# Kernel tuning notes

Measured on AMD Instinct MI355X. Metric: run time of the kernel, lower is better.

Reference implementation:

```python
import jax, jax.numpy as jnp
import numpy as np

DIM = 1024
HEADS = 16
DIM_HEAD = 64
INNER = HEADS * DIM_HEAD  # 1024
SCALE = DIM_HEAD ** -0.5


def setup_inputs() -> dict:
    key = jax.random.key(0)
    ks = jax.random.split(key, 5)
    B, N = 4, 2048
    x = jax.random.normal(ks[0], (B, N, DIM), dtype=jnp.float32)
    # torch Linear weights are [out, in]; store transposed [in, out] for x @ W
    s = 1.0 / np.sqrt(DIM)
    Wq = jax.random.uniform(ks[1], (DIM, INNER), minval=-s, maxval=s, dtype=jnp.float32)
    Wkv = jax.random.uniform(ks[2], (DIM, 2 * INNER), minval=-s, maxval=s, dtype=jnp.float32)
    so = 1.0 / np.sqrt(INNER)
    Wo = jax.random.uniform(ks[3], (INNER, DIM), minval=-so, maxval=so, dtype=jnp.float32)
    bo = jax.random.uniform(ks[4], (DIM,), minval=-so, maxval=so, dtype=jnp.float32)
    return {"x": x, "Wq": Wq, "Wkv": Wkv, "Wo": Wo, "bo": bo}


def reference(x, Wq, Wkv, Wo, bo):
    B, N, _ = x.shape
    q = x @ Wq                      # [B, N, INNER]
    kv = x @ Wkv                    # [B, N, 2*INNER]
    k, v = jnp.split(kv, 2, axis=-1)

    def split_heads(t):
        return t.reshape(B, N, HEADS, DIM_HEAD).transpose(0, 2, 1, 3)  # [B,H,N,D]

    q, k, v = split_heads(q) * SCALE, split_heads(k), split_heads(v)
    sim = jnp.einsum('bhid,bhjd->bhij', q, k)  # [B,H,N,N]
    mask_value = -jnp.finfo(sim.dtype).max
    # causal: mask strictly-upper triangle (triu with offset j-i+1 = 1)
    causal_mask = jnp.triu(jnp.ones((N, N), dtype=bool), k=1)
    sim = jnp.where(causal_mask[None, None, :, :], mask_value, sim)
    attn = jax.nn.softmax(sim, axis=-1)
    out = jnp.einsum('bhij,bhjd->bhid', attn, v)            # [B,H,N,D]
    out = out.transpose(0, 2, 1, 3).reshape(B, N, INNER)    # [B,N,INNER]
    return out @ Wo + bo
```

## Files before the change

### kernel.cpp

```cpp
#include <hip/hip_runtime.h>

typedef unsigned short u16;
typedef __bf16 bf16x8 __attribute__((ext_vector_type(8)));
typedef float floatx4 __attribute__((ext_vector_type(4)));
typedef unsigned as1_u32 __attribute__((address_space(1)));
typedef unsigned as3_u32 __attribute__((address_space(3)));

__device__ inline u16 f2bf(float f) {
    unsigned int u = __builtin_bit_cast(unsigned int, f);
    u += 0x7fffu + ((u >> 16) & 1u);
    return (u16)(u >> 16);
}
__device__ inline floatx4 mfma16(bf16x8 a, bf16x8 b, floatx4 c) {
    return __builtin_amdgcn_mfma_f32_16x16x32_bf16(a, b, c, 0, 0, 0);
}
__device__ inline void gld16(const u16* g, u16* l) {
    __builtin_amdgcn_global_load_lds((const as1_u32*)g, (as3_u32*)l, 16, 0, 0);
}
__device__ inline unsigned permpack(float lo, float hi) {
    return __builtin_amdgcn_perm(__builtin_bit_cast(unsigned, hi),
                                 __builtin_bit_cast(unsigned, lo), 0x07060302u);
}

#define NSEQ 2048
#define DIM  1024
#define HEADS 16
#define DHEAD 64
#define QSCALE 0.18033688f
#define CSHIFT 4.328085f

__device__ inline void transpose_tile(const float* __restrict__ src,
                                      u16* __restrict__ dst, int ncols,
                                      int n0, int k0, int t) {
    __shared__ u16 tile[64][72];
    #pragma unroll
    for (int rr = 0; rr < 4; rr++) {
        const int k = (t >> 4) + rr * 16;
        const int n = (t & 15) * 4;
        float4 v = *(const float4*)&src[(size_t)(k0 + k) * ncols + n0 + n];
        tile[n + 0][k] = f2bf(v.x); tile[n + 1][k] = f2bf(v.y);
        tile[n + 2][k] = f2bf(v.z); tile[n + 3][k] = f2bf(v.w);
    }
    __syncthreads();
    #pragma unroll
    for (int ww = 0; ww < 2; ww++) {
        const int idx = t + ww * 256;
        const int n = idx >> 3, g = idx & 7;
        u16 tmp[8] __attribute__((aligned(16)));
        #pragma unroll
        for (int i = 0; i < 8; i++) tmp[i] = tile[n][g * 8 + i];
        *(uint4*)&dst[(size_t)(n0 + n) * 1024 + k0 + g * 8] = *(const uint4*)tmp;
    }
}

__global__ __launch_bounds__(256) void prep_fused(
    const float* __restrict__ x,  u16* __restrict__ xb,
    const float* __restrict__ Wq, const float* __restrict__ Wkv,
    u16* __restrict__ Wt)
{
    const int bid = blockIdx.x;
    const int t = threadIdx.x;
    if (bid < 4096) {
        const size_t i = ((size_t)bid * 256 + t) * 8;
        float4 a = *(const float4*)&x[i];
        float4 b = *(const float4*)&x[i + 4];
        u16 o[8] __attribute__((aligned(16)));
        o[0] = f2bf(a.x); o[1] = f2bf(a.y); o[2] = f2bf(a.z); o[3] = f2bf(a.w);
        o[4] = f2bf(b.x); o[5] = f2bf(b.y); o[6] = f2bf(b.z); o[7] = f2bf(b.w);
        *(uint4*)&xb[i] = *(const uint4*)o;
    } else if (bid < 4352) {
        const int v = bid - 4096;
        transpose_tile(Wq, Wt, 1024, (v & 15) * 64, (v >> 4) * 64, t);
    } else {
        const int v = bid - 4352;
        transpose_tile(Wkv, Wt + (size_t)1024 * 1024, 2048, (v & 31) * 64, (v >> 5) * 64, t);
    }
}

__global__ __launch_bounds__(256) void transpose_conv(const float* __restrict__ src,
                                                      u16* __restrict__ dst, int ncols) {
    transpose_tile(src, dst, ncols, blockIdx.x * 64, blockIdx.y * 64, threadIdx.x);
}

__global__ __launch_bounds__(256) void qkv_gemm_v3(
    const u16* __restrict__ xb, const u16* __restrict__ Wt,
    u16* __restrict__ q_ws, u16* __restrict__ k_ws, u16* __restrict__ v_ws)
{
    __shared__ u16 a0[128 * 32], a1[128 * 32];
    __shared__ u16 b0[128 * 32], b1[128 * 32];

    const int n0 = blockIdx.x * 128;
    const int m0 = blockIdx.y * 128;
    const int t = threadIdx.x, lane = t & 63, w = t >> 6;
    const int wr = w >> 1, wc = w & 1;
    const int quad = lane >> 4, l16 = lane & 15;
    const int lrow = lane >> 2, lk = (lane & 3) * 8;

    floatx4 acc[4][4];
    #pragma unroll
    for (int i = 0; i < 4; i++)
        #pragma unroll
        for (int j = 0; j < 4; j++) acc[i][j] = floatx4{0.f, 0.f, 0.f, 0.f};

    for (int k0 = 0; k0 < DIM; k0 += 64) {
        __syncthreads();
        #pragma unroll
        for (int hh = 0; hh < 2; hh++) {
            const int row = w * 32 + hh * 16;
            const size_t ga = (size_t)(m0 + row + lrow) * DIM + k0 + lk;
            const size_t gb = (size_t)(n0 + row + lrow) * DIM + k0 + lk;
            gld16(&xb[ga],      &a0[row * 32]);
            gld16(&xb[ga + 32], &a1[row * 32]);
            gld16(&Wt[gb],      &b0[row * 32]);
            gld16(&Wt[gb + 32], &b1[row * 32]);
        }
        __syncthreads();

        #pragma unroll
        for (int ks = 0; ks < 2; ks++) {
            const u16* al = ks ? a1 : a0;
            const u16* bl = ks ? b1 : b0;
            bf16x8 af[4], bf[4];
            #pragma unroll
            for (int i = 0; i < 4; i++)
                af[i] = *(const bf16x8*)&al[(wr * 64 + i * 16 + l16) * 32 + quad * 8];
            #pragma unroll
            for (int j = 0; j < 4; j++)
                bf[j] = *(const bf16x8*)&bl[(wc * 64 + j * 16 + l16) * 32 + quad * 8];
            #pragma unroll
            for (int i = 0; i < 4; i++)
                #pragma unroll
                for (int j = 0; j < 4; j++)
                    acc[i][j] = mfma16(af[i], bf[j], acc[i][j]);
        }
    }

    const int seg = n0 >> 10;
    #pragma unroll
    for (int j = 0; j < 4; j++) {
        const int n  = n0 + wc * 64 + j * 16 + l16;
        const int nn = n & 1023;
        const int h  = nn >> 6, d = nn & 63;
        #pragma unroll
        for (int i = 0; i < 4; i++) {
            const int mb = m0 + wr * 64 + i * 16 + quad * 4;
            const int b = mb >> 11, ib = mb & (NSEQ - 1);
            if (seg == 0) {
                #pragma unroll
                for (int r = 0; r < 4; r++)
                    q_ws[(((size_t)(b * HEADS + h)) * NSEQ + ib + r) * DHEAD + d] =
                        f2bf(acc[i][j][r] * QSCALE);
            } else if (seg == 1) {
                #pragma unroll
                for (int r = 0; r < 4; r++)
                    k_ws[(((size_t)(b * HEADS + h)) * NSEQ + ib + r) * DHEAD + d] =
                        f2bf(acc[i][j][r]);
            } else {
                u16 tmp[4] __attribute__((aligned(8)));
                #pragma unroll
                for (int r = 0; r < 4; r++) tmp[r] = f2bf(acc[i][j][r]);
                *(uint2*)&v_ws[(((size_t)(b * HEADS + h)) * DHEAD + d) * NSEQ + ib] =
                    *(const uint2*)tmp;
            }
        }
    }
}

__global__ __launch_bounds__(256) void attn_v8(
    const u16* __restrict__ q_ws, const u16* __restrict__ k_ws,
    const u16* __restrict__ v_ws, u16* __restrict__ attn_ws)
{
    __shared__ u16 kds[2][64 * 64];
    __shared__ u16 vds[2][64 * 64];
    __shared__ u16 p_lds[4 * 2048];

    const int bid = blockIdx.x;
    const int bh  = bid & 63;
    const int t16 = 15 - (bid >> 6);
    const int i0  = t16 * 128;
    const int b   = bh >> 4, h = bh & 15;

    const u16* qb = q_ws + (size_t)bh * NSEQ * DHEAD;
    const u16* kb = k_ws + (size_t)bh * NSEQ * DHEAD;
    const u16* vb = v_ws + (size_t)bh * DHEAD * NSEQ;

    const int t    = threadIdx.x;
    const int lane = t & 63, w = t >> 6;
    const int quad = lane >> 4, l16 = lane & 15;

    const int srow8 = lane >> 3;
    const int chunk = (lane & 7) ^ srow8;
    const int krow  = w * 16 + srow8;
    const size_t koff = (size_t)krow * DHEAD + chunk * 8;
    const size_t voff = (size_t)krow * NSEQ + chunk * 8;
    u16* klbase = (u16*)&kds[0][0] + w * 1024;
    u16* vlbase = (u16*)&vds[0][0] + w * 1024;
    const int sw = (l16 & 7);

    bf16x8 qf[2][2];
    #pragma unroll
    for (int rf = 0; rf < 2; rf++)
        #pragma unroll
        for (int dg = 0; dg < 2; dg++)
            qf[rf][dg] = *(const bf16x8*)&qb[(size_t)(i0 + rf * 64 + w * 16 + l16) * DHEAD
                                             + dg * 32 + quad * 8];

    floatx4 l4[2] = {floatx4{0.f,0.f,0.f,0.f}, floatx4{0.f,0.f,0.f,0.f}};
    floatx4 acc[2][4];
    #pragma unroll
    for (int rf = 0; rf < 2; rf++)
        #pragma unroll
        for (int dg = 0; dg < 4; dg++) acc[rf][dg] = floatx4{0.f, 0.f, 0.f, 0.f};

    const int jt_max = 2 * t16 + 1;

    gld16(&kb[koff],             klbase);
    gld16(&kb[koff + 8 * DHEAD], klbase + 512);
    gld16(&vb[voff],             vlbase);
    gld16(&vb[voff + 8 * NSEQ],  vlbase + 512);

    for (int jt = 0; jt <= jt_max; jt++) {
        const int cur = jt & 1;
        __syncthreads();

        if (jt < jt_max) {
            const size_t j64 = (size_t)(jt + 1) * 64;
            const int nb = (cur ^ 1) * 4096;
            gld16(&kb[j64 * DHEAD + koff],             klbase + nb);
            gld16(&kb[j64 * DHEAD + koff + 8 * DHEAD], klbase + nb + 512);
            gld16(&vb[j64 + voff],                     vlbase + nb);
            gld16(&vb[j64 + voff + 8 * NSEQ],          vlbase + nb + 512);
        }

        const u16* kl = &kds[cur][0];
        const u16* vl = &vds[cur][0];
        const int j0 = jt * 64;

        floatx4 s[2][4];
        #pragma unroll
        for (int rf = 0; rf < 2; rf++)
            #pragma unroll
            for (int g = 0; g < 4; g++)
                s[rf][g] = floatx4{-CSHIFT, -CSHIFT, -CSHIFT, -CSHIFT};
        __builtin_amdgcn_s_setprio(1);
        #pragma unroll
        for (int dg = 0; dg < 2; dg++)
            #pragma unroll
            for (int g = 0; g < 4; g++) {
                bf16x8 kf = *(const bf16x8*)&kl[(g * 16 + l16) * 64
                                                + (((dg * 4 + quad) ^ sw) * 8)];
                s[0][g] = mfma16(kf, qf[0][dg], s[0][g]);
                s[1][g] = mfma16(kf, qf[1][dg], s[1][g]);
            }
        __builtin_amdgcn_s_setprio(0);

        #pragma unroll
        for (int rf = 0; rf < 2; rf++) {
            const int imin = i0 + rf * 64 + w * 16;
            if (j0 + 63 > imin) {
                const int i = imin + l16;
                #pragma unroll
                for (int g = 0; g < 4; g++) {
                    const int jb = j0 + g * 16 + quad * 4;
                    #pragma unroll
                    for (int r = 0; r < 4; r++)
                        if (jb + r > i) s[rf][g][r] = -1e30f;
                }
            }
        }

        #pragma unroll
        for (int rf = 0; rf < 2; rf++) {
            #pragma unroll
            for (int g = 0; g < 4; g++) {
                #pragma unroll
                for (int r = 0; r < 4; r++)
                    s[rf][g][r] = __builtin_amdgcn_exp2f(s[rf][g][r]);
                l4[rf] += s[rf][g];
                uint2 pk;
                pk.x = permpack(s[rf][g][0], s[rf][g][1]);
                pk.y = permpack(s[rf][g][2], s[rf][g][3]);
                const int c = 2 * g + (quad >> 1);
                *(uint2*)&p_lds[w * 2048 + rf * 1024 + (c >> 2) * 512 + (c & 3) * 128
                                + l16 * 8 + (quad & 1) * 4] = pk;
            }
        }
        asm volatile("s_waitcnt lgkmcnt(0)" ::: "memory");

        __builtin_amdgcn_s_setprio(1);
        #pragma unroll
        for (int jg = 0; jg < 2; jg++) {
            bf16x8 pf0 = *(const bf16x8*)&p_lds[w * 2048 + jg * 512 + quad * 128 + l16 * 8];
            bf16x8 pf1 = *(const bf16x8*)&p_lds[w * 2048 + 1024 + jg * 512 + quad * 128 + l16 * 8];
            #pragma unroll
            for (int dg = 0; dg < 4; dg++) {
                bf16x8 vf = *(const bf16x8*)&vl[(dg * 16 + l16) * 64
                                                + (((jg * 4 + quad) ^ sw) * 8)];
                acc[0][dg] = mfma16(pf0, vf, acc[0][dg]);
                acc[1][dg] = mfma16(pf1, vf, acc[1][dg]);
            }
        }
        __builtin_amdgcn_s_setprio(0);
    }

    #pragma unroll
    for (int rf = 0; rf < 2; rf++) {
        float l_ln = (l4[rf][0] + l4[rf][1]) + (l4[rf][2] + l4[rf][3]);
        l_ln += __shfl_xor(l_ln, 16);
        l_ln += __shfl_xor(l_ln, 32);
        float linv[4];
        #pragma unroll
        for (int r = 0; r < 4; r++)
            linv[r] = 1.0f / __shfl(l_ln, quad * 4 + r);
        #pragma unroll
        for (int dg = 0; dg < 4; dg++)
            #pragma unroll
            for (int r = 0; r < 4; r++) {
                const float o = acc[rf][dg][r] * linv[r];
                const int i = i0 + rf * 64 + w * 16 + quad * 4 + r;
                attn_ws[(((size_t)(b * NSEQ + i)) * HEADS + h) * DHEAD + dg * 16 + l16] =
                    f2bf(o);
            }
    }
}

__global__ __launch_bounds__(256) void out_gemm_v3(
    const u16* __restrict__ attn, const u16* __restrict__ Wot,
    const float* __restrict__ bo, float* __restrict__ out)
{
    __shared__ u16 a0[128 * 32], a1[128 * 32];
    __shared__ u16 b0[128 * 32], b1[128 * 32];

    const int n0 = blockIdx.x * 128;
    const int m0 = blockIdx.y * 128;
    const int t = threadIdx.x, lane = t & 63, w = t >> 6;
    const int wr = w >> 1, wc = w & 1;
    const int quad = lane >> 4, l16 = lane & 15;
    const int lrow = lane >> 2, lk = (lane & 3) * 8;

    floatx4 acc[4][4];
    #pragma unroll
    for (int i = 0; i < 4; i++)
        #pragma unroll
        for (int j = 0; j < 4; j++) acc[i][j] = floatx4{0.f, 0.f, 0.f, 0.f};

    for (int k0 = 0; k0 < DIM; k0 += 64) {
        __syncthreads();
        #pragma unroll
        for (int hh = 0; hh < 2; hh++) {
            const int row = w * 32 + hh * 16;
            const size_t ga = (size_t)(m0 + row + lrow) * DIM + k0 + lk;
            const size_t gb = (size_t)(n0 + row + lrow) * DIM + k0 + lk;
            gld16(&attn[ga],      &a0[row * 32]);
            gld16(&attn[ga + 32], &a1[row * 32]);
            gld16(&Wot[gb],       &b0[row * 32]);
            gld16(&Wot[gb + 32],  &b1[row * 32]);
        }
        __syncthreads();

        #pragma unroll
        for (int ks = 0; ks < 2; ks++) {
            const u16* al = ks ? a1 : a0;
            const u16* bl = ks ? b1 : b0;
            bf16x8 af[4], bf[4];
            #pragma unroll
            for (int i = 0; i < 4; i++)
                af[i] = *(const bf16x8*)&al[(wr * 64 + i * 16 + l16) * 32 + quad * 8];
            #pragma unroll
            for (int j = 0; j < 4; j++)
                bf[j] = *(const bf16x8*)&bl[(wc * 64 + j * 16 + l16) * 32 + quad * 8];
            #pragma unroll
            for (int i = 0; i < 4; i++)
                #pragma unroll
                for (int j = 0; j < 4; j++)
                    acc[i][j] = mfma16(af[i], bf[j], acc[i][j]);
        }
    }

    #pragma unroll
    for (int j = 0; j < 4; j++) {
        const int n = n0 + wc * 64 + j * 16 + l16;
        const float bias = bo[n];
        #pragma unroll
        for (int i = 0; i < 4; i++) {
            #pragma unroll
            for (int r = 0; r < 4; r++) {
                const int m = m0 + wr * 64 + i * 16 + quad * 4 + r;
                out[(size_t)m * DIM + n] = acc[i][j][r] + bias;
            }
        }
    }
}

extern "C" void kernel_launch(void* const* d_in, const int* in_sizes, int n_in,
                              void* d_out, int out_size, void* d_ws, size_t ws_size,
                              hipStream_t stream) {
    const float* x   = (const float*)d_in[0];
    const float* Wq  = (const float*)d_in[1];
    const float* Wkv = (const float*)d_in[2];
    const float* Wo  = (const float*)d_in[3];
    const float* bo  = (const float*)d_in[4];

    u16* q_ws = (u16*)d_out;
    u16* xb   = (u16*)d_out + (size_t)8388608;

    u16* ws   = (u16*)d_ws;
    u16* k_ws = ws;
    u16* v_ws = ws + (size_t)8388608;
    u16* a_ws = ws + (size_t)16777216;
    u16* Wt   = a_ws;
    u16* Wot  = k_ws;

    prep_fused<<<4864, 256, 0, stream>>>(x, xb, Wq, Wkv, Wt);
    qkv_gemm_v3<<<dim3(24, 64), 256, 0, stream>>>(xb, Wt, q_ws, k_ws, v_ws);
    attn_v8<<<dim3(1024), 256, 0, stream>>>(q_ws, k_ws, v_ws, a_ws);
    transpose_conv<<<dim3(16, 16), 256, 0, stream>>>(Wo, Wot, 1024);
    out_gemm_v3<<<dim3(8, 64), 256, 0, stream>>>(a_ws, Wot, bo, (float*)d_out);
}
```

Measured before the change: 252.8 us.

## Triple-buffer QKV GEMM with async LDS loads, XOR swizzle, and 256x128 tiles

Rewrites the QKV projection GEMM to use 512-thread blocks on 256x128 output tiles with a three-stage global-to-LDS pipeline. Tile loads for two steps ahead are issued while computing the current one, with explicit vmcnt waits and scheduling barriers. LDS rows are XOR-swizzled to avoid bank conflicts, and MFMA issue priority is raised. This aims to hide global load latency and cut synchronization per K-step. In exchange it uses much more LDS per block and fewer blocks.

```diff
diff --git a/kernel.cpp b/kernel.cpp
--- a/kernel.cpp
+++ b/kernel.cpp
@@ -82,19 +82,23 @@
     transpose_tile(src, dst, ncols, blockIdx.x * 64, blockIdx.y * 64, threadIdx.x);
 }
 
-__global__ __launch_bounds__(256) void qkv_gemm_v3(
+__global__ __launch_bounds__(512, 2) void qkv_gemm_v4(
     const u16* __restrict__ xb, const u16* __restrict__ Wt,
     u16* __restrict__ q_ws, u16* __restrict__ k_ws, u16* __restrict__ v_ws)
 {
-    __shared__ u16 a0[128 * 32], a1[128 * 32];
-    __shared__ u16 b0[128 * 32], b1[128 * 32];
+    __shared__ u16 As[3][256 * 64];
+    __shared__ u16 Bs[3][128 * 64];
 
     const int n0 = blockIdx.x * 128;
-    const int m0 = blockIdx.y * 128;
+    const int m0 = blockIdx.y * 256;
     const int t = threadIdx.x, lane = t & 63, w = t >> 6;
     const int wr = w >> 1, wc = w & 1;
     const int quad = lane >> 4, l16 = lane & 15;
-    const int lrow = lane >> 2, lk = (lane & 3) * 8;
+
+    const int srow = lane >> 3;
+    const int c8   = (lane & 7) ^ srow;
+    const size_t gA = (size_t)(m0 + w * 8 + srow) * DIM + c8 * 8;
+    const size_t gB = (size_t)(n0 + w * 8 + srow) * DIM + c8 * 8;
 
     floatx4 acc[4][4];
     #pragma unroll
@@ -102,63 +106,85 @@
         #pragma unroll
         for (int j = 0; j < 4; j++) acc[i][j] = floatx4{0.f, 0.f, 0.f, 0.f};
 
-    for (int k0 = 0; k0 < DIM; k0 += 64) {
-        __syncthreads();
-        #pragma unroll
-        for (int hh = 0; hh < 2; hh++) {
-            const int row = w * 32 + hh * 16;
-            const size_t ga = (size_t)(m0 + row + lrow) * DIM + k0 + lk;
-            const size_t gb = (size_t)(n0 + row + lrow) * DIM + k0 + lk;
-            gld16(&xb[ga],      &a0[row * 32]);
-            gld16(&xb[ga + 32], &a1[row * 32]);
-            gld16(&Wt[gb],      &b0[row * 32]);
-            gld16(&Wt[gb + 32], &b1[row * 32]);
-        }
-        __syncthreads();
-
+#define STAGE_QKV(tt, buf) do {                                            \
+    const size_t k0s = (size_t)(tt) * 64;                                  \
+    u16* ab = &As[buf][w * 512];                                           \
+    u16* bb = &Bs[buf][w * 512];                                           \
+    gld16(&xb[gA + k0s],             ab);                                  \
+    gld16(&xb[gA + k0s +  64 * DIM], ab + 4096);                           \
+    gld16(&xb[gA + k0s + 128 * DIM], ab + 8192);                           \
+    gld16(&xb[gA + k0s + 192 * DIM], ab + 12288);                          \
+    gld16(&Wt[gB + k0s],             bb);                                  \
+    gld16(&Wt[gB + k0s +  64 * DIM], bb + 4096);                           \
+} while (0)
+
+    STAGE_QKV(0, 0);
+    STAGE_QKV(1, 1);
+
+    int cur = 0, nxt = 2;
+    for (int tt = 0; tt < 16; tt++) {
+        __builtin_amdgcn_sched_barrier(0);
+        __builtin_amdgcn_s_barrier();
+        __builtin_amdgcn_sched_barrier(0);
+        if (tt < 14) STAGE_QKV(tt + 2, nxt);
+        __builtin_amdgcn_sched_barrier(0);
+        if (tt < 14)       asm volatile("s_waitcnt vmcnt(12)" ::: "memory");
+        else if (tt == 14) asm volatile("s_waitcnt vmcnt(6)"  ::: "memory");
+        else               asm volatile("s_waitcnt vmcnt(0)"  ::: "memory");
+        __builtin_amdgcn_sched_barrier(0);
+        __builtin_amdgcn_s_barrier();
+        __builtin_amdgcn_sched_barrier(0);
+
+        const u16* al = &As[cur][0];
+        const u16* bl = &Bs[cur][0];
         #pragma unroll
         for (int ks = 0; ks < 2; ks++) {
-            const u16* al = ks ? a1 : a0;
-            const u16* bl = ks ? b1 : b0;
             bf16x8 af[4], bf[4];
             #pragma unroll
-            for (int i = 0; i < 4; i++)
-                af[i] = *(const bf16x8*)&al[(wr * 64 + i * 16 + l16) * 32 + quad * 8];
-            #pragma unroll
-            for (int j = 0; j < 4; j++)
-                bf[j] = *(const bf16x8*)&bl[(wc * 64 + j * 16 + l16) * 32 + quad * 8];
-            #pragma unroll
-            for (int i = 0; i < 4; i++)
-                #pragma unroll
-                for (int j = 0; j < 4; j++)
-                    acc[i][j] = mfma16(af[i], bf[j], acc[i][j]);
-        }
-    }
+            for (int mi = 0; mi < 4; mi++)
+                af[mi] = *(const bf16x8*)&al[(wr * 64 + mi * 16 + l16) * 64
+                                             + (((ks * 4 + quad) ^ (l16 & 7)) * 8)];
+            #pragma unroll
+            for (int nj = 0; nj < 4; nj++)
+                bf[nj] = *(const bf16x8*)&bl[(wc * 64 + nj * 16 + l16) * 64
+                                             + (((ks * 4 + quad) ^ (l16 & 7)) * 8)];
+            __builtin_amdgcn_s_setprio(1);
+            #pragma unroll
+            for (int mi = 0; mi < 4; mi++)
+                #pragma unroll
+                for (int nj = 0; nj < 4; nj++)
+                    acc[mi][nj] = mfma16(af[mi], bf[nj], acc[mi][nj]);
+            __builtin_amdgcn_s_setprio(0);
+        }
+        cur = (cur == 2) ? 0 : cur + 1;
+        nxt = (nxt == 2) ? 0 : nxt + 1;
+    }
+#undef STAGE_QKV
 
     const int seg = n0 >> 10;
     #pragma unroll
-    for (int j = 0; j < 4; j++) {
-        const int n  = n0 + wc * 64 + j * 16 + l16;
+    for (int nj = 0; nj < 4; nj++) {
+        const int n  = n0 + wc * 64 + nj * 16 + l16;
         const int nn = n & 1023;
         const int h  = nn >> 6, d = nn & 63;
         #pragma unroll
-        for (int i = 0; i < 4; i++) {
-            const int mb = m0 + wr * 64 + i * 16 + quad * 4;
+        for (int mi = 0; mi < 4; mi++) {
+            const int mb = m0 + wr * 64 + mi * 16 + quad * 4;
             const int b = mb >> 11, ib = mb & (NSEQ - 1);
             if (seg == 0) {
                 #pragma unroll
                 for (int r = 0; r < 4; r++)
                     q_ws[(((size_t)(b * HEADS + h)) * NSEQ + ib + r) * DHEAD + d] =
-                        f2bf(acc[i][j][r] * QSCALE);
+                        f2bf(acc[mi][nj][r] * QSCALE);
             } else if (seg == 1) {
                 #pragma unroll
                 for (int r = 0; r < 4; r++)
                     k_ws[(((size_t)(b * HEADS + h)) * NSEQ + ib + r) * DHEAD + d] =
-                        f2bf(acc[i][j][r]);
+                        f2bf(acc[mi][nj][r]);
             } else {
                 u16 tmp[4] __attribute__((aligned(8)));
                 #pragma unroll
-                for (int r = 0; r < 4; r++) tmp[r] = f2bf(acc[i][j][r]);
+                for (int r = 0; r < 4; r++) tmp[r] = f2bf(acc[mi][nj][r]);
                 *(uint2*)&v_ws[(((size_t)(b * HEADS + h)) * DHEAD + d) * NSEQ + ib] =
                     *(const uint2*)tmp;
             }
@@ -412,7 +438,7 @@
     u16* Wot  = k_ws;
 
     prep_fused<<<4864, 256, 0, stream>>>(x, xb, Wq, Wkv, Wt);
-    qkv_gemm_v3<<<dim3(24, 64), 256, 0, stream>>>(xb, Wt, q_ws, k_ws, v_ws);
+    qkv_gemm_v4<<<dim3(24, 32), 512, 0, stream>>>(xb, Wt, q_ws, k_ws, v_ws);
     attn_v8<<<dim3(1024), 256, 0, stream>>>(q_ws, k_ws, v_ws, a_ws);
     transpose_conv<<<dim3(16, 16), 256, 0, stream>>>(Wo, Wot, 1024);
     out_gemm_v3<<<dim3(8, 64), 256, 0, stream>>>(a_ws, Wot, bo, (float*)d_out);
```

Result: slower. 261.8 us (+3.6%).
